# Performance work log

Measured on AMD Instinct MI355X. Metric: run time of the kernel, lower is better.

## Reference

```python
import jax, jax.numpy as jnp
import numpy as np
import math

KSIZE = 5

def setup_inputs() -> dict:
    key = jax.random.key(0)
    ks = jax.random.split(key, 4)
    B, Cp, h, w = 4, 80, 64, 64
    Cf, H, W = 256, 128, 128
    Cc = 64
    pred = jax.random.normal(ks[0], (B, Cp, h, w), dtype=jnp.float32)
    feat = jax.random.normal(ks[1], (B, Cf, H, W), dtype=jnp.float32)
    # hr_compress: 1x1 conv, xavier-like scale; bias zero (matches _reset_parameters)
    w_compress = jax.random.normal(ks[2], (Cc, Cf), dtype=jnp.float32) * (1.0 / np.sqrt(Cf))
    b_compress = jnp.zeros((Cc,), dtype=jnp.float32)
    # content_encoder: 3x3 conv, std=0.001 init; bias zero
    w_enc = jax.random.normal(ks[3], (KSIZE * KSIZE, Cc, 3, 3), dtype=jnp.float32) * 0.001
    b_enc = jnp.zeros((KSIZE * KSIZE,), dtype=jnp.float32)
    return dict(pred=pred, feat=feat, w_compress=w_compress, b_compress=b_compress,
                w_enc=w_enc, b_enc=b_enc)


def _carafe(x, normed_mask, k, up):
    # x: (b, c, h, w) low-res; normed_mask: (b, k*k, H, W) softmax over k*k
    b, c, h, w = x.shape
    _, _, H, W = normed_mask.shape
    pad = k // 2
    px = jnp.pad(x, ((0, 0), (0, 0), (pad, pad), (pad, pad)), mode='reflect')
    # F.unfold ordering: kernel offsets row-major (ki, kj) -> (b, c, k*k, h, w)
    patches = jnp.stack([px[:, :, i:i + h, j:j + w]
                         for i in range(k) for j in range(k)], axis=2)
    # nearest-neighbor upsample by `up` then crop to (H, W): out[i,j] = in[i//up, j//up]
    iy = jnp.arange(H) // up
    ix = jnp.arange(W) // up
    pu = patches[:, :, :, iy[:, None], ix[None, :]]  # (b, c, k*k, H, W)
    return jnp.sum(pu * normed_mask[:, None, :, :, :], axis=2)  # (b, c, H, W)


def reference(pred, feat, w_compress, b_compress, w_enc, b_enc):
    B, Cf, H, W = feat.shape
    _, Cp, h, w = pred.shape
    k = KSIZE
    up = max(math.ceil(H / float(h)), math.ceil(W / float(w)))
    # hr_compress: 1x1 conv as channel contraction
    guide = jnp.einsum('bchw,oc->bohw', feat, w_compress) + b_compress[None, :, None, None]
    # content_encoder: 3x3 SAME conv -> k*k mask logits
    raw = jax.lax.conv_general_dilated(guide, w_enc, (1, 1), 'SAME',
                                       dimension_numbers=('NCHW', 'OIHW', 'NCHW'))
    raw = raw + b_enc[None, :, None, None]
    # kernel normalizer: softmax over the k*k kernel positions (groups=1)
    mask = jax.nn.softmax(raw.reshape(B, 1, k * k, H, W), axis=2).reshape(B, k * k, H, W)
    return _carafe(pred, mask, k, up)
```

## Files before the change

### kernel.cpp

```cpp
#include <hip/hip_runtime.h>
#include <hip/hip_bf16.h>

#define BB   4
#define CF   256
#define CC   64
#define CP   80
#define HH   128
#define WW   128
#define KK   25
#define NPIX 16384

typedef __attribute__((ext_vector_type(8))) short short8v;
typedef __attribute__((ext_vector_type(4))) short short4v;
typedef __attribute__((ext_vector_type(4))) float f32x4;
typedef __attribute__((ext_vector_type(2))) float f32x2;

static __device__ __forceinline__ short f2bf(float f) {
  __hip_bfloat16 h = __float2bfloat16(f);
  return *reinterpret_cast<short*>(&h);
}

__global__ __launch_bounds__(256) void k_compress(
    const float* __restrict__ feat, const float* __restrict__ wc,
    const float* __restrict__ bc, const float* __restrict__ we,
    short* __restrict__ guide, short* __restrict__ web) {
  __shared__ short Al[32 * 520];
  __shared__ short Bl[64 * 72];
  const int tid = threadIdx.x;
  const int bx = blockIdx.x;
  const int b = bx >> 8;
  const int y = (bx >> 1) & 127;
  const int x0 = (bx & 1) << 6;

  {
    int j = bx * 256 + tid;
    if (j < 9 * 32 * 64) {
      int tap = j >> 11, kk = (j >> 6) & 31, c = j & 63;
      float v = (kk < KK) ? we[(kk * 64 + c) * 9 + tap] : 0.f;
      web[j] = f2bf(v);
    }
  }

#pragma unroll
  for (int t = 0; t < 8; ++t) {
    int idx = tid + t * 256;
    int o = idx >> 5, c8 = idx & 31;
    const f32x4* src = (const f32x4*)(wc + o * CF + c8 * 8);
    f32x4 v0 = src[0], v1 = src[1];
    short8v h;
    h[0] = f2bf(v0.x); h[1] = f2bf(v0.y); h[2] = f2bf(v0.z); h[3] = f2bf(v0.w);
    h[4] = f2bf(v1.x); h[5] = f2bf(v1.y); h[6] = f2bf(v1.z); h[7] = f2bf(v1.w);
    int cblk = c8 >> 2, lh4 = c8 & 3;
    *(short8v*)(Al + (cblk * 4 + lh4) * 520 + o * 8) = h;
  }

  const int wave = tid >> 6, l = tid & 63;
  const int l15 = l & 15, lh = l >> 4;
  const int px_s = tid & 63;
  const int c_s = (tid >> 6) << 4;
  const float* fb = feat + (size_t)b * CF * NPIX + y * WW + x0;

  f32x4 acc[4];
#pragma unroll
  for (int m = 0; m < 4; ++m) acc[m] = (f32x4){0.f, 0.f, 0.f, 0.f};

  for (int c0 = 0; c0 < CF; c0 += 64) {
    if (c0) __syncthreads();
    float v[16];
#pragma unroll
    for (int i = 0; i < 16; ++i)
      v[i] = fb[(size_t)(c0 + c_s + i) * NPIX + px_s];
    short8v h0, h1;
#pragma unroll
    for (int e = 0; e < 8; ++e) { h0[e] = f2bf(v[e]); h1[e] = f2bf(v[8 + e]); }
    *(short8v*)(Bl + px_s * 72 + c_s) = h0;
    *(short8v*)(Bl + px_s * 72 + c_s + 8) = h1;
    __syncthreads();
#pragma unroll
    for (int ks = 0; ks < 64; ks += 32) {
      const int cblk = (c0 + ks) >> 5;
      short8v bfr = *(const short8v*)(Bl + (wave * 16 + l15) * 72 + ks + lh * 8);
#pragma unroll
      for (int m = 0; m < 4; ++m) {
        short8v a = *(const short8v*)(Al + (cblk * 4 + lh) * 520 +
                                      (m * 16 + l15) * 8);
        acc[m] = __builtin_amdgcn_mfma_f32_16x16x32_bf16(a, bfr, acc[m], 0, 0, 0);
      }
    }
  }

  const int px = wave * 16 + l15;
  short* gb = guide + ((size_t)((b * HH + y) * WW + x0 + px)) * CC;
#pragma unroll
  for (int m = 0; m < 4; ++m) {
    short4v o;
#pragma unroll
    for (int r = 0; r < 4; ++r) {
      int c = m * 16 + lh * 4 + r;
      o[r] = f2bf(acc[m][r] + bc[c]);
    }
    *(short4v*)(gb + m * 16 + lh * 4) = o;
  }
}

__global__ __launch_bounds__(256) void k_conv(
    const short* __restrict__ guide, const short* __restrict__ web,
    const float* __restrict__ be, float* __restrict__ maskq) {
  __shared__ short Gl[10 * 10 * 72];
  __shared__ short webF[36 * 528];
  const int tid = threadIdx.x;
  const int bx = blockIdx.x;
  const int b = bx >> 8;
  const int t = bx & 255;
  const int y0 = (t >> 4) << 3, x0 = (t & 15) << 3;
  const int wave = tid >> 6, l = tid & 63;
  const int l15 = l & 15, lh = l >> 4;

#pragma unroll
  for (int it = 0; it < 9; ++it) {
    int i = it * 256 + tid;
    int c8 = i & 7, kk = (i >> 3) & 31, tap = i >> 8;
    short8v v = *(const short8v*)(web + i * 8);
    int frag = tap * 4 + ((kk >> 4) << 1) + (c8 >> 2);
    int lane = (kk & 15) | ((c8 & 3) << 4);
    *(short8v*)(webF + frag * 528 + lane * 8) = v;
  }

  for (int idx = tid; idx < 10 * 10 * 8; idx += 256) {
    int yp = idx / 80;
    int rem = idx - yp * 80;
    int xp = rem >> 3, cq = (rem & 7) << 3;
    int gy = y0 - 1 + yp, gx = x0 - 1 + xp;
    short8v v = {0, 0, 0, 0, 0, 0, 0, 0};
    if (gy >= 0 && gy < HH && gx >= 0 && gx < WW)
      v = *(const short8v*)(guide + ((size_t)((b * HH + gy) * WW + gx)) * CC + cq);
    *(short8v*)(Gl + (yp * 10 + xp) * 72 + cq) = v;
  }
  __syncthreads();

  const int r_ = wave * 2 + (l15 >> 3);
  const int cx = l15 & 7;
  f32x4 acc0 = {0.f, 0.f, 0.f, 0.f}, acc1 = {0.f, 0.f, 0.f, 0.f};
#pragma unroll
  for (int tap = 0; tap < 9; ++tap) {
    const int dy = tap / 3, dx = tap - dy * 3;
#pragma unroll
    for (int ks32 = 0; ks32 < 2; ++ks32) {
      short8v a0 = *(const short8v*)(webF + (tap * 4 + ks32) * 528 + l * 8);
      short8v a1 = *(const short8v*)(webF + (tap * 4 + 2 + ks32) * 528 + l * 8);
      short8v bf = *(const short8v*)(Gl + ((r_ + dy) * 10 + cx + dx) * 72 +
                                     ks32 * 32 + lh * 8);
      acc0 = __builtin_amdgcn_mfma_f32_16x16x32_bf16(a0, bf, acc0, 0, 0, 0);
      acc1 = __builtin_amdgcn_mfma_f32_16x16x32_bf16(a1, bf, acc1, 0, 0, 0);
    }
  }

  float sv[8];
#pragma unroll
  for (int r = 0; r < 4; ++r) {
    int kk0 = lh * 4 + r;
    sv[r] = acc0[r] + be[kk0];
    int kk1 = 16 + lh * 4 + r;
    sv[4 + r] = (kk1 < KK) ? (acc1[r] + be[kk1]) : -1e30f;
  }
  float mx = sv[0];
#pragma unroll
  for (int i = 1; i < 8; ++i) mx = fmaxf(mx, sv[i]);
  mx = fmaxf(mx, __shfl_xor(mx, 16));
  mx = fmaxf(mx, __shfl_xor(mx, 32));
  float s = 0.f;
#pragma unroll
  for (int i = 0; i < 8; ++i) {
    sv[i] = __expf(sv[i] - mx);
    s += sv[i];
  }
  s += __shfl_xor(s, 16);
  s += __shfl_xor(s, 32);
  float inv = 1.f / s;

  const int Y = y0 + r_, X = x0 + cx;
  const size_t pxoff = (size_t)(Y << 7) + X;
  f32x4 o0 = {sv[0] * inv, sv[1] * inv, sv[2] * inv, sv[3] * inv};
  *(f32x4*)(maskq + ((((size_t)(b * 7 + lh)) << 14) + pxoff) * 4) = o0;
  if (lh < 3) {
    f32x4 o1 = {sv[4] * inv, sv[5] * inv, sv[6] * inv, sv[7] * inv};
    *(f32x4*)(maskq + ((((size_t)(b * 7 + 4 + lh)) << 14) + pxoff) * 4) = o1;
  }
}

__global__ __launch_bounds__(256) void k_carafe3(
    const float* __restrict__ pred, const float* __restrict__ maskq,
    float* __restrict__ out) {
  __shared__ float Pl[64 * 50];
  __shared__ float Msk[64 * 30];
  const int tid = threadIdx.x;
  const int bx = blockIdx.x;
  const int half = bx & 1;
  const int t = (bx >> 1) & 255;
  const int b = bx >> 9;
  const int y0 = (t >> 4) << 3, x0 = (t & 15) << 3;

  const int ylo = (y0 >> 1) - 2, xlo = (x0 >> 1) - 2;
#pragma unroll
  for (int it = 0; it < 10; ++it) {
    int idx = it * 256 + tid;
    int c = idx >> 6;
    int cell = idx & 63;
    int r = cell >> 3, cl = cell & 7;
    int ry = ylo + r;
    ry = ry < 0 ? -ry : (ry > 63 ? 126 - ry : ry);
    int rx = xlo + cl;
    rx = rx < 0 ? -rx : (rx > 63 ? 126 - rx : rx);
    int gg = c / 5, cc = c - gg * 5;
    Pl[cell * 50 + gg * 6 + cc] =
        pred[(((size_t)(b * CP + half * 40 + c)) << 12) + (ry << 6) + rx];
  }

  for (int idx = tid; idx < 448; idx += 256) {
    int q = idx >> 6, pxl = idx & 63;
    int yy = pxl >> 3, xx = pxl & 7;
    f32x4 v = *(const f32x4*)(maskq + ((((size_t)(b * 7 + q)) << 14) +
                                       ((size_t)((y0 + yy) << 7)) + x0 + xx) * 4);
    float* dst = Msk + pxl * 30 + q * 4;
    *(f32x2*)dst = (f32x2){v.x, v.y};
    *(f32x2*)(dst + 2) = (f32x2){v.z, v.w};
  }
  __syncthreads();

  const int g = tid >> 5;
  const int pr = tid & 31;
  const int pry = pr >> 2, prx = pr & 3;
  const int Y = y0 + pry, X = x0 + prx * 2;
  float m[2][KK];
#pragma unroll
  for (int dxp = 0; dxp < 2; ++dxp) {
    const float* mb = Msk + (pry * 8 + prx * 2 + dxp) * 30;
#pragma unroll
    for (int q = 0; q < 7; ++q) {
      f32x2 lo = *(const f32x2*)(mb + q * 4);
      f32x2 hi = *(const f32x2*)(mb + q * 4 + 2);
      int kk = q * 4;
      m[dxp][kk] = lo.x;
      if (kk + 1 < KK) m[dxp][kk + 1] = lo.y;
      if (kk + 2 < KK) m[dxp][kk + 2] = hi.x;
      if (kk + 3 < KK) m[dxp][kk + 3] = hi.y;
    }
  }

  float acc[5][2];
#pragma unroll
  for (int cc = 0; cc < 5; ++cc) { acc[cc][0] = 0.f; acc[cc][1] = 0.f; }

  const float* Pbase = Pl + ((pry >> 1) * 8 + prx) * 50 + g * 6;
#pragma unroll
  for (int i = 0; i < 5; ++i)
#pragma unroll
    for (int j = 0; j < 5; ++j) {
      const float* P = Pbase + (i * 8 + j) * 50;
      f32x2 p01 = *(const f32x2*)(P);
      f32x2 p23 = *(const f32x2*)(P + 2);
      float p4 = P[4];
      float m0 = m[0][i * 5 + j], m1 = m[1][i * 5 + j];
      acc[0][0] += p01.x * m0; acc[0][1] += p01.x * m1;
      acc[1][0] += p01.y * m0; acc[1][1] += p01.y * m1;
      acc[2][0] += p23.x * m0; acc[2][1] += p23.x * m1;
      acc[3][0] += p23.y * m0; acc[3][1] += p23.y * m1;
      acc[4][0] += p4    * m0; acc[4][1] += p4    * m1;
    }

#pragma unroll
  for (int cc = 0; cc < 5; ++cc) {
    float* ob = out + (((size_t)(b * CP + half * 40 + g * 5 + cc)) << 14) +
                Y * WW + X;
    f32x2 v2 = {acc[cc][0], acc[cc][1]};
    *(f32x2*)ob = v2;
  }
}

extern "C" void kernel_launch(void* const* d_in, const int* in_sizes, int n_in,
                              void* d_out, int out_size, void* d_ws,
                              size_t ws_size, hipStream_t stream) {
  (void)in_sizes; (void)n_in; (void)out_size; (void)ws_size;
  const float* pred = (const float*)d_in[0];
  const float* feat = (const float*)d_in[1];
  const float* wc   = (const float*)d_in[2];
  const float* bc   = (const float*)d_in[3];
  const float* we   = (const float*)d_in[4];
  const float* be   = (const float*)d_in[5];
  float* out = (float*)d_out;

  char* ws = (char*)d_ws;
  short* guide = (short*)ws;
  short* web   = (short*)(ws + 8388608);
  float* maskq = (float*)(ws + 8388608 + 36864);

  hipLaunchKernelGGL(k_compress, dim3(1024), dim3(256), 0, stream,
                     feat, wc, bc, we, guide, web);
  hipLaunchKernelGGL(k_conv, dim3(1024), dim3(256), 0, stream,
                     guide, web, be, maskq);
  hipLaunchKernelGGL(k_carafe3, dim3(2048), dim3(256), 0, stream,
                     pred, maskq, out);
}
```

Before: 47.62 us.

## Fuse mask conv/softmax with CARAFE reassembly into one kernel via shared memory

Result: faster. 45.47 us (-4.5%).

```diff
diff --git a/kernel.cpp b/kernel.cpp
--- a/kernel.cpp
+++ b/kernel.cpp
@@ -103,11 +103,15 @@
   }
 }
 
-__global__ __launch_bounds__(256) void k_conv(
+__global__ __launch_bounds__(256) void k_fused(
     const short* __restrict__ guide, const short* __restrict__ web,
-    const float* __restrict__ be, float* __restrict__ maskq) {
-  __shared__ short Gl[10 * 10 * 72];
-  __shared__ short webF[36 * 528];
+    const float* __restrict__ be, const float* __restrict__ pred,
+    float* __restrict__ out) {
+  __shared__ char smem[36864 + 14400];
+  short* webF = (short*)smem;
+  short* Gl = (short*)(smem + 36864);
+  float* Ml = (float*)smem;
+  float* Pl = (float*)(smem + 36864);
   const int tid = threadIdx.x;
   const int bx = blockIdx.x;
   const int b = bx >> 8;
@@ -123,7 +127,7 @@
     short8v v = *(const short8v*)(web + i * 8);
     int frag = tap * 4 + ((kk >> 4) << 1) + (c8 >> 2);
     int lane = (kk & 15) | ((c8 & 3) << 4);
-    *(short8v*)(webF + frag * 528 + lane * 8) = v;
+    *(short8v*)(webF + frag * 512 + lane * 8) = v;
   }
 
   for (int idx = tid; idx < 10 * 10 * 8; idx += 256) {
@@ -146,8 +150,8 @@
     const int dy = tap / 3, dx = tap - dy * 3;
 #pragma unroll
     for (int ks32 = 0; ks32 < 2; ++ks32) {
-      short8v a0 = *(const short8v*)(webF + (tap * 4 + ks32) * 528 + l * 8);
-      short8v a1 = *(const short8v*)(webF + (tap * 4 + 2 + ks32) * 528 + l * 8);
+      short8v a0 = *(const short8v*)(webF + (tap * 4 + ks32) * 512 + l * 8);
+      short8v a1 = *(const short8v*)(webF + (tap * 4 + 2 + ks32) * 512 + l * 8);
       short8v bf = *(const short8v*)(Gl + ((r_ + dy) * 10 + cx + dx) * 72 +
                                      ks32 * 32 + lh * 8);
       acc0 = __builtin_amdgcn_mfma_f32_16x16x32_bf16(a0, bf, acc0, 0, 0, 0);
@@ -178,102 +182,88 @@
   s += __shfl_xor(s, 32);
   float inv = 1.f / s;
 
-  const int Y = y0 + r_, X = x0 + cx;
-  const size_t pxoff = (size_t)(Y << 7) + X;
-  f32x4 o0 = {sv[0] * inv, sv[1] * inv, sv[2] * inv, sv[3] * inv};
-  *(f32x4*)(maskq + ((((size_t)(b * 7 + lh)) << 14) + pxoff) * 4) = o0;
-  if (lh < 3) {
-    f32x4 o1 = {sv[4] * inv, sv[5] * inv, sv[6] * inv, sv[7] * inv};
-    *(f32x4*)(maskq + ((((size_t)(b * 7 + 4 + lh)) << 14) + pxoff) * 4) = o1;
-  }
-}
-
-__global__ __launch_bounds__(256) void k_carafe3(
-    const float* __restrict__ pred, const float* __restrict__ maskq,
-    float* __restrict__ out) {
-  __shared__ float Pl[64 * 50];
-  __shared__ float Msk[64 * 30];
-  const int tid = threadIdx.x;
-  const int bx = blockIdx.x;
-  const int half = bx & 1;
-  const int t = (bx >> 1) & 255;
-  const int b = bx >> 9;
-  const int y0 = (t >> 4) << 3, x0 = (t & 15) << 3;
-
-  const int ylo = (y0 >> 1) - 2, xlo = (x0 >> 1) - 2;
-#pragma unroll
-  for (int it = 0; it < 10; ++it) {
-    int idx = it * 256 + tid;
-    int c = idx >> 6;
-    int cell = idx & 63;
-    int r = cell >> 3, cl = cell & 7;
-    int ry = ylo + r;
-    ry = ry < 0 ? -ry : (ry > 63 ? 126 - ry : ry);
-    int rx = xlo + cl;
-    rx = rx < 0 ? -rx : (rx > 63 ? 126 - rx : rx);
-    int gg = c / 5, cc = c - gg * 5;
-    Pl[cell * 50 + gg * 6 + cc] =
-        pred[(((size_t)(b * CP + half * 40 + c)) << 12) + (ry << 6) + rx];
-  }
-
-  for (int idx = tid; idx < 448; idx += 256) {
-    int q = idx >> 6, pxl = idx & 63;
-    int yy = pxl >> 3, xx = pxl & 7;
-    f32x4 v = *(const f32x4*)(maskq + ((((size_t)(b * 7 + q)) << 14) +
-                                       ((size_t)((y0 + yy) << 7)) + x0 + xx) * 4);
-    float* dst = Msk + pxl * 30 + q * 4;
-    *(f32x2*)dst = (f32x2){v.x, v.y};
-    *(f32x2*)(dst + 2) = (f32x2){v.z, v.w};
-  }
   __syncthreads();
+
+  {
+    int pxm = wave * 16 + l15;
+#pragma unroll
+    for (int r = 0; r < 4; ++r) {
+      Ml[pxm * 30 + lh * 4 + r] = sv[r] * inv;
+      if (lh < 3) Ml[pxm * 30 + 16 + lh * 4 + r] = sv[4 + r] * inv;
+    }
+  }
 
   const int g = tid >> 5;
   const int pr = tid & 31;
   const int pry = pr >> 2, prx = pr & 3;
   const int Y = y0 + pry, X = x0 + prx * 2;
+  const int ylo = (y0 >> 1) - 2, xlo = (x0 >> 1) - 2;
+
   float m[2][KK];
-#pragma unroll
-  for (int dxp = 0; dxp < 2; ++dxp) {
-    const float* mb = Msk + (pry * 8 + prx * 2 + dxp) * 30;
-#pragma unroll
-    for (int q = 0; q < 7; ++q) {
-      f32x2 lo = *(const f32x2*)(mb + q * 4);
-      f32x2 hi = *(const f32x2*)(mb + q * 4 + 2);
-      int kk = q * 4;
-      m[dxp][kk] = lo.x;
-      if (kk + 1 < KK) m[dxp][kk + 1] = lo.y;
-      if (kk + 2 < KK) m[dxp][kk + 2] = hi.x;
-      if (kk + 3 < KK) m[dxp][kk + 3] = hi.y;
-    }
-  }
-
-  float acc[5][2];
-#pragma unroll
-  for (int cc = 0; cc < 5; ++cc) { acc[cc][0] = 0.f; acc[cc][1] = 0.f; }
-
   const float* Pbase = Pl + ((pry >> 1) * 8 + prx) * 50 + g * 6;
-#pragma unroll
-  for (int i = 0; i < 5; ++i)
-#pragma unroll
-    for (int j = 0; j < 5; ++j) {
-      const float* P = Pbase + (i * 8 + j) * 50;
-      f32x2 p01 = *(const f32x2*)(P);
-      f32x2 p23 = *(const f32x2*)(P + 2);
-      float p4 = P[4];
-      float m0 = m[0][i * 5 + j], m1 = m[1][i * 5 + j];
-      acc[0][0] += p01.x * m0; acc[0][1] += p01.x * m1;
-      acc[1][0] += p01.y * m0; acc[1][1] += p01.y * m1;
-      acc[2][0] += p23.x * m0; acc[2][1] += p23.x * m1;
-      acc[3][0] += p23.y * m0; acc[3][1] += p23.y * m1;
-      acc[4][0] += p4    * m0; acc[4][1] += p4    * m1;
-    }
-
-#pragma unroll
-  for (int cc = 0; cc < 5; ++cc) {
-    float* ob = out + (((size_t)(b * CP + half * 40 + g * 5 + cc)) << 14) +
-                Y * WW + X;
-    f32x2 v2 = {acc[cc][0], acc[cc][1]};
-    *(f32x2*)ob = v2;
+
+  for (int half = 0; half < 2; ++half) {
+#pragma unroll
+    for (int it = 0; it < 10; ++it) {
+      int idx = it * 256 + tid;
+      int c = idx >> 6;
+      int cell = idx & 63;
+      int r = cell >> 3, cl = cell & 7;
+      int ry = ylo + r;
+      ry = ry < 0 ? -ry : (ry > 63 ? 126 - ry : ry);
+      int rx = xlo + cl;
+      rx = rx < 0 ? -rx : (rx > 63 ? 126 - rx : rx);
+      int gg = c / 5, cc = c - gg * 5;
+      Pl[cell * 50 + gg * 6 + cc] =
+          pred[(((size_t)(b * CP + half * 40 + c)) << 12) + (ry << 6) + rx];
+    }
+    __syncthreads();
+
+    if (half == 0) {
+#pragma unroll
+      for (int dxp = 0; dxp < 2; ++dxp) {
+        const float* mb = Ml + (pry * 8 + prx * 2 + dxp) * 30;
+#pragma unroll
+        for (int q = 0; q < 7; ++q) {
+          f32x2 lo = *(const f32x2*)(mb + q * 4);
+          f32x2 hi = *(const f32x2*)(mb + q * 4 + 2);
+          int kk = q * 4;
+          m[dxp][kk] = lo.x;
+          if (kk + 1 < KK) m[dxp][kk + 1] = lo.y;
+          if (kk + 2 < KK) m[dxp][kk + 2] = hi.x;
+          if (kk + 3 < KK) m[dxp][kk + 3] = hi.y;
+        }
+      }
+    }
+
+    float acc[5][2];
+#pragma unroll
+    for (int cc = 0; cc < 5; ++cc) { acc[cc][0] = 0.f; acc[cc][1] = 0.f; }
+
+#pragma unroll
+    for (int i = 0; i < 5; ++i)
+#pragma unroll
+      for (int j = 0; j < 5; ++j) {
+        const float* P = Pbase + (i * 8 + j) * 50;
+        f32x2 p01 = *(const f32x2*)(P);
+        f32x2 p23 = *(const f32x2*)(P + 2);
+        float p4 = P[4];
+        float m0 = m[0][i * 5 + j], m1 = m[1][i * 5 + j];
+        acc[0][0] += p01.x * m0; acc[0][1] += p01.x * m1;
+        acc[1][0] += p01.y * m0; acc[1][1] += p01.y * m1;
+        acc[2][0] += p23.x * m0; acc[2][1] += p23.x * m1;
+        acc[3][0] += p23.y * m0; acc[3][1] += p23.y * m1;
+        acc[4][0] += p4    * m0; acc[4][1] += p4    * m1;
+      }
+
+#pragma unroll
+    for (int cc = 0; cc < 5; ++cc) {
+      float* ob = out + (((size_t)(b * CP + half * 40 + g * 5 + cc)) << 14) +
+                  Y * WW + X;
+      f32x2 v2 = {acc[cc][0], acc[cc][1]};
+      *(f32x2*)ob = v2;
+    }
+    if (half == 0) __syncthreads();
   }
 }
 
@@ -292,12 +282,9 @@
   char* ws = (char*)d_ws;
   short* guide = (short*)ws;
   short* web   = (short*)(ws + 8388608);
-  float* maskq = (float*)(ws + 8388608 + 36864);
 
   hipLaunchKernelGGL(k_compress, dim3(1024), dim3(256), 0, stream,
                      feat, wc, bc, we, guide, web);
-  hipLaunchKernelGGL(k_conv, dim3(1024), dim3(256), 0, stream,
-                     guide, web, be, maskq);
-  hipLaunchKernelGGL(k_carafe3, dim3(2048), dim3(256), 0, stream,
-                     pred, maskq, out);
-}
+  hipLaunchKernelGGL(k_fused, dim3(1024), dim3(256), 0, stream,
+                     guide, web, be, pred, out);
+}
```
